# Optimization experiments

Measured on AMD Instinct MI355X. Metric: run time of the kernel, lower is better.

## Reference

```python
import jax, jax.numpy as jnp
import numpy as np

B, K, D = 262144, 512, 3


def setup_inputs() -> dict:
    key = jax.random.key(0)
    k_ze, k_e = jax.random.split(key)
    ze = jax.random.normal(k_ze, (B, D, 1), dtype=jnp.float32)
    e = jax.random.normal(k_e, (K, D), dtype=jnp.float32)  # codebook, learned param
    return {"ze": ze, "e": e}


def reference(ze, e):
    # ze: (B, D, 1), e: (K, D)
    # Per-dimension L2 distance to every codebook entry: (B, K, D)
    l2diff = (jnp.transpose(ze, (0, 2, 1)) - e[None, :, :]) ** 2
    # Independent argmin over the codebook axis for each of the D dims: (B, D)
    z = jnp.argmin(l2diff, axis=1)
    # Gather per-dimension codebook scalars: zq[b, d] = e[z[b, d], d]
    zq = e[z, jnp.arange(D)]  # (B, D)
    return (z, zq)
```

## Files before the change

### kernel.cpp

```cpp
#include <hip/hip_runtime.h>

#define B_TOTAL 262144
#define K_CB    512
#define D_DIM   3
#define BLOCK   256

__device__ __forceinline__ unsigned int mono32(unsigned int u) {
    unsigned int m = (u & 0x80000000u) ? 0xFFFFFFFFu : 0x80000000u;
    return u ^ m;
}

__global__ __launch_bounds__(BLOCK) void rank_kernel(
    const float* __restrict__ e, float* __restrict__ ws_val, int* __restrict__ ws_idx)
{
    const int d    = blockIdx.x >> 1;
    const int half = blockIdx.x & 1;
    const int tid  = threadIdx.x;

    __shared__ unsigned long long key[K_CB];
    __shared__ float              val[K_CB];

    for (int k = tid; k < K_CB; k += BLOCK) {
        float v = e[k * D_DIM + d];
        key[k] = ((unsigned long long)mono32(__float_as_uint(v)) << 32) | (unsigned int)k;
        val[k] = v;
    }
    __syncthreads();

    const int i = half * BLOCK + tid;
    const unsigned long long mykey = key[i];
    int rank = 0;
    #pragma unroll 8
    for (int j = 0; j < K_CB; ++j)
        rank += (key[j] < mykey) ? 1 : 0;

    ws_val[d * K_CB + rank] = val[i];
    ws_idx[d * K_CB + rank] = i;
}

__global__ __launch_bounds__(BLOCK) void vq_search_kernel(
    const float* __restrict__ ze,
    const float* __restrict__ ws_val, const int* __restrict__ ws_idx,
    float* __restrict__ z_out, float* __restrict__ zq_out)
{
    __shared__ float sval[D_DIM][K_CB];
    __shared__ int   sidx[D_DIM][K_CB];

    const int tid = threadIdx.x;
    for (int i = tid; i < D_DIM * K_CB; i += BLOCK) {
        ((float*)sval)[i] = ws_val[i];
        ((int*)sidx)[i]   = ws_idx[i];
    }
    __syncthreads();

    const int b = blockIdx.x * BLOCK + tid;
    const float xs[D_DIM] = { ze[b * 3 + 0], ze[b * 3 + 1], ze[b * 3 + 2] };

    #pragma unroll
    for (int d = 0; d < D_DIM; ++d) {
        const float xv = xs[d];

        int lo = -1, hi = K_CB;
        #pragma unroll
        for (int it = 0; it < 9; ++it) {
            int mid = (lo + hi) >> 1;
            bool le = sval[d][mid] <= xv;
            lo = le ? mid : lo;
            hi = le ? hi : mid;
        }

        float dl = 3.402823466e38f, vl = 0.0f; int il = 0;
        if (lo >= 0) {
            vl = sval[d][lo];
            int p = lo;
            while (p > 0 && sval[d][p - 1] == vl) --p;
            il = sidx[d][p];
            float t = xv - vl;
            dl = t * t;
        }
        float dr = 3.402823466e38f, vr = 0.0f; int ir = 0;
        if (lo < K_CB - 1) {
            vr = sval[d][lo + 1];
            ir = sidx[d][lo + 1];
            float t = xv - vr;
            dr = t * t;
        }

        const bool pickR = (dr < dl) || ((dr == dl) && (ir < il));
        z_out [b * 3 + d] = (float)(pickR ? ir : il);
        zq_out[b * 3 + d] = pickR ? vr : vl;
    }
}

extern "C" void kernel_launch(void* const* d_in, const int* in_sizes, int n_in,
                              void* d_out, int out_size, void* d_ws, size_t ws_size,
                              hipStream_t stream) {
    const float* ze = (const float*)d_in[0];
    const float* e  = (const float*)d_in[1];
    float* z_out  = (float*)d_out;
    float* zq_out = z_out + (size_t)B_TOTAL * D_DIM;

    float* ws_val = (float*)d_ws;
    int*   ws_idx = (int*)(ws_val + D_DIM * K_CB);

    rank_kernel     <<<D_DIM * 2,       BLOCK, 0, stream>>>(e, ws_val, ws_idx);
    vq_search_kernel<<<B_TOTAL / BLOCK, BLOCK, 0, stream>>>(ze, ws_val, ws_idx,
                                                            z_out, zq_out);
}
```

Before: 71.20 us.

## Add uniform-grid lookup table to narrow binary search range per query

The rank kernel now also builds, per dimension, a 2049-entry table that maps uniform bins over [-4,4] to positions in the sorted codebook. The search kernel loads this table into shared memory and uses it to bound the binary search, so most queries need only a few iterations instead of nine. This costs extra shared memory (about 12KB more per block) and a larger preload per block, which may reduce occupancy. The rank kernel also drops from six blocks to three by ranking two keys per thread.

```diff
diff --git a/kernel.cpp b/kernel.cpp
--- a/kernel.cpp
+++ b/kernel.cpp
@@ -4,52 +4,79 @@
 #define K_CB    512
 #define D_DIM   3
 #define BLOCK   256
+#define LUT_N   2048
+#define LUT_E   (LUT_N + 1)
+#define LUT_PAD 2052
 
 __device__ __forceinline__ unsigned int mono32(unsigned int u) {
     unsigned int m = (u & 0x80000000u) ? 0xFFFFFFFFu : 0x80000000u;
     return u ^ m;
 }
 
-__global__ __launch_bounds__(BLOCK) void rank_kernel(
-    const float* __restrict__ e, float* __restrict__ ws_val, int* __restrict__ ws_idx)
+__global__ __launch_bounds__(BLOCK) void rank_lut_kernel(
+    const float* __restrict__ e, float* __restrict__ ws_val,
+    int* __restrict__ ws_idx, unsigned short* __restrict__ ws_lut)
 {
-    const int d    = blockIdx.x >> 1;
-    const int half = blockIdx.x & 1;
-    const int tid  = threadIdx.x;
+    const int d   = blockIdx.x;
+    const int tid = threadIdx.x;
 
     __shared__ unsigned long long key[K_CB];
-    __shared__ float              val[K_CB];
+    __shared__ float vals[K_CB];
+    __shared__ float sval[K_CB];
+    __shared__ int   sidx[K_CB];
 
     for (int k = tid; k < K_CB; k += BLOCK) {
         float v = e[k * D_DIM + d];
-        key[k] = ((unsigned long long)mono32(__float_as_uint(v)) << 32) | (unsigned int)k;
-        val[k] = v;
+        vals[k] = v;
+        key[k]  = ((unsigned long long)mono32(__float_as_uint(v)) << 32)
+                | (unsigned int)k;
     }
     __syncthreads();
 
-    const int i = half * BLOCK + tid;
-    const unsigned long long mykey = key[i];
-    int rank = 0;
+    const unsigned long long my0 = key[tid], my1 = key[tid + BLOCK];
+    int r0 = 0, r1 = 0;
     #pragma unroll 8
-    for (int j = 0; j < K_CB; ++j)
-        rank += (key[j] < mykey) ? 1 : 0;
+    for (int j = 0; j < K_CB; ++j) {
+        unsigned long long kj = key[j];
+        r0 += (kj < my0) ? 1 : 0;
+        r1 += (kj < my1) ? 1 : 0;
+    }
+    sval[r0] = vals[tid];         sidx[r0] = tid;
+    sval[r1] = vals[tid + BLOCK]; sidx[r1] = tid + BLOCK;
+    __syncthreads();
 
-    ws_val[d * K_CB + rank] = val[i];
-    ws_idx[d * K_CB + rank] = i;
+    for (int k = tid; k < K_CB; k += BLOCK) {
+        ws_val[d * K_CB + k] = sval[k];
+        ws_idx[d * K_CB + k] = sidx[k];
+    }
+
+    for (int t = tid; t < LUT_E; t += BLOCK) {
+        float edge = -4.0f + (float)t * 0.00390625f;
+        int lo = 0, hi = K_CB;
+        while (lo < hi) { int mid = (lo + hi) >> 1;
+                          if (sval[mid] <= edge) lo = mid + 1; else hi = mid; }
+        ws_lut[d * LUT_PAD + t] = (unsigned short)lo;
+    }
 }
 
 __global__ __launch_bounds__(BLOCK) void vq_search_kernel(
     const float* __restrict__ ze,
     const float* __restrict__ ws_val, const int* __restrict__ ws_idx,
+    const unsigned int* __restrict__ ws_lut_u32,
     float* __restrict__ z_out, float* __restrict__ zq_out)
 {
-    __shared__ float sval[D_DIM][K_CB];
-    __shared__ int   sidx[D_DIM][K_CB];
+    __shared__ float          sval[D_DIM][K_CB];
+    __shared__ int            sidx[D_DIM][K_CB];
+    __shared__ unsigned short slut[D_DIM][LUT_PAD];
 
     const int tid = threadIdx.x;
-    for (int i = tid; i < D_DIM * K_CB; i += BLOCK) {
-        ((float*)sval)[i] = ws_val[i];
-        ((int*)sidx)[i]   = ws_idx[i];
+    {
+        const float4* gv = (const float4*)ws_val; float4* lv = (float4*)sval;
+        for (int i = tid; i < D_DIM * K_CB / 4; i += BLOCK) lv[i] = gv[i];
+        const int4* gi = (const int4*)ws_idx; int4* li = (int4*)sidx;
+        for (int i = tid; i < D_DIM * K_CB / 4; i += BLOCK) li[i] = gi[i];
+        unsigned int* ll = (unsigned int*)slut;
+        for (int i = tid; i < D_DIM * LUT_PAD / 2; i += BLOCK) ll[i] = ws_lut_u32[i];
     }
     __syncthreads();
 
@@ -60,9 +87,15 @@
     for (int d = 0; d < D_DIM; ++d) {
         const float xv = xs[d];
 
-        int lo = -1, hi = K_CB;
-        #pragma unroll
-        for (int it = 0; it < 9; ++it) {
+        float tf = floorf((xv + 4.0f) * 256.0f);
+        int t = (int)fmaxf(fminf(tf, 1.0e6f), -1.0e6f);
+
+        int tl = t - 1;
+        int lo = (tl < 0) ? -1
+               : (int)slut[d][tl > LUT_N ? LUT_N : tl] - 1;
+        int hi = (t >= LUT_N - 2) ? K_CB : (int)slut[d][t + 2];
+
+        while (hi - lo > 1) {
             int mid = (lo + hi) >> 1;
             bool le = sval[d][mid] <= xv;
             lo = le ? mid : lo;
@@ -75,15 +108,15 @@
             int p = lo;
             while (p > 0 && sval[d][p - 1] == vl) --p;
             il = sidx[d][p];
-            float t = xv - vl;
-            dl = t * t;
+            float tt = xv - vl;
+            dl = tt * tt;
         }
         float dr = 3.402823466e38f, vr = 0.0f; int ir = 0;
         if (lo < K_CB - 1) {
             vr = sval[d][lo + 1];
             ir = sidx[d][lo + 1];
-            float t = xv - vr;
-            dr = t * t;
+            float tt = xv - vr;
+            dr = tt * tt;
         }
 
         const bool pickR = (dr < dl) || ((dr == dl) && (ir < il));
@@ -100,10 +133,12 @@
     float* z_out  = (float*)d_out;
     float* zq_out = z_out + (size_t)B_TOTAL * D_DIM;
 
-    float* ws_val = (float*)d_ws;
-    int*   ws_idx = (int*)(ws_val + D_DIM * K_CB);
+    float*          ws_val = (float*)d_ws;
+    int*            ws_idx = (int*)(ws_val + D_DIM * K_CB);
+    unsigned short* ws_lut = (unsigned short*)(ws_idx + D_DIM * K_CB);
 
-    rank_kernel     <<<D_DIM * 2,       BLOCK, 0, stream>>>(e, ws_val, ws_idx);
+    rank_lut_kernel <<<D_DIM,           BLOCK, 0, stream>>>(e, ws_val, ws_idx, ws_lut);
     vq_search_kernel<<<B_TOTAL / BLOCK, BLOCK, 0, stream>>>(ze, ws_val, ws_idx,
+                                                            (const unsigned int*)ws_lut,
                                                             z_out, zq_out);
 }
```

Result: slower. 79.57 us (+11.8%).
